# Kernel tuning notes

Measured on AMD Instinct MI355X. Metric: run time of the kernel, lower is better.

Reference implementation:

```python
import jax, jax.numpy as jnp
import numpy as np

B, C, L = 4, 16, 1024
U_SELF, U_CROSS, HID = 32, 16, 128
WIDTH = 128
EPS = 1e-5
LN_EPS = 1e-14


def _band_mask(n, w):
    j = jnp.arange(n)
    lo = j - w // 2
    hi = lo + w
    i = j[:, None]
    return (lo <= i) & (i < hi)  # mask[i, j]: query i attends key j


def _layernorm(x, gamma, beta):
    # channel-first LN over dim 1; gamma/beta shape (C, 1)
    mean = jnp.mean(x, 1, keepdims=True)
    var = jnp.mean((x - mean) ** 2, 1, keepdims=True) + LN_EPS
    return (x - mean) / jnp.sqrt(var) * gamma + beta


def _self_attn(x, Wt, Wx, bh, Wa, ba):
    xt = x.transpose(0, 2, 1)                                # (B,L,C)
    q = xt @ Wt                                              # (B,L,U)
    k = xt @ Wx                                              # (B,L,U)
    h = jnp.tanh(q[:, :, None, :] + k[:, None, :, :] + bh)   # (B,L,L,U)
    e = jnp.squeeze(h @ Wa, -1) + ba                         # (B,L,L)
    e = jnp.exp(e - jnp.max(e, -1, keepdims=True))
    e = jnp.where(_band_mask(e.shape[1], WIDTH), e, 0.0)
    a = e / (jnp.sum(e, -1, keepdims=True) + EPS)
    v = a @ xt                                               # (B,L,C)
    return v.transpose(0, 2, 1)


def _ff(x, W1, b1, W2, b2):
    xt = x.transpose(0, 2, 1)
    h = jax.nn.relu(xt @ W1 + b1)
    return (h @ W2 + b2).transpose(0, 2, 1)


def _transformer(x, Wt, Wx, bh, Wa, ba, g1, be1, W1, b1, W2, b2, g2, be2):
    y = _layernorm(x + _self_attn(x, Wt, Wx, bh, Wa, ba), g1, be1)
    return _layernorm(y + _ff(y, W1, b1, W2, b2), g2, be2)


def _cross(y1, y2, Wq, Wk, Wv):
    y1t = y1.transpose(0, 2, 1)
    y2t = y2.transpose(0, 2, 1)
    q = y1t @ Wq
    k = y2t @ Wk
    v = y2t @ Wv                                             # (B,L,Uc)
    e = (q @ k.transpose(0, 2, 1)) * (1.0 / np.float32(np.sqrt(U_CROSS)))
    e = jnp.where(_band_mask(e.shape[-1], WIDTH), e, -jnp.inf)
    a = jax.nn.softmax(e, -1)
    return (a @ v).transpose(0, 2, 1)                        # (B,Uc,L)


def _forward(x1, x2, t1, t2, cw, top):
    y1 = _transformer(x1, *t1)
    y2 = _transformer(x2, *t2)
    g1, be1, W1, b1, W2, b2, g2, be2 = top
    y = _layernorm(y1 + _cross(y1, y2, *cw), g1, be1)
    return _layernorm(y + _ff(y, W1, b1, W2, b2), g2, be2)


def setup_inputs() -> dict:
    key = jax.random.key(0)
    ks = iter(jax.random.split(key, 64))
    u = lambda shape: jax.random.uniform(next(ks), shape, jnp.float32, -0.02, 0.02)
    n = lambda shape: jax.random.normal(next(ks), shape, jnp.float32) * 0.05
    d = {"x1": jax.random.normal(next(ks), (B, C, L), jnp.float32),
         "x2": jax.random.normal(next(ks), (B, C, L), jnp.float32)}
    for p in ("t1", "t2"):
        d[p + "_Wt"] = u((C, U_SELF)); d[p + "_Wx"] = u((C, U_SELF))
        d[p + "_bh"] = jnp.zeros(U_SELF)
        d[p + "_Wa"] = u((U_SELF, 1)); d[p + "_ba"] = jnp.zeros(1)
        d[p + "_g1"] = jnp.ones((C, 1)); d[p + "_be1"] = jnp.zeros((C, 1))
        d[p + "_W1"] = n((C, HID)); d[p + "_b1"] = jnp.zeros(HID)
        d[p + "_W2"] = n((HID, C)); d[p + "_b2"] = jnp.zeros(C)
        d[p + "_g2"] = jnp.ones((C, 1)); d[p + "_be2"] = jnp.zeros((C, 1))
    d["ca_Wq"] = u((C, U_CROSS)); d["ca_Wk"] = u((C, U_CROSS)); d["ca_Wv"] = u((C, U_CROSS))
    d["g1"] = jnp.ones((C, 1)); d["be1"] = jnp.zeros((C, 1))
    d["W1"] = n((C, HID)); d["b1"] = jnp.zeros(HID)
    d["W2"] = n((HID, C)); d["b2"] = jnp.zeros(C)
    d["g2"] = jnp.ones((C, 1)); d["be2"] = jnp.zeros((C, 1))
    return d


def reference(x1, x2, t1_Wt, t1_Wx, t1_bh, t1_Wa, t1_ba, t1_g1, t1_be1, t1_W1, t1_b1, t1_W2, t1_b2, t1_g2, t1_be2, t2_Wt, t2_Wx, t2_bh, t2_Wa, t2_ba, t2_g1, t2_be1, t2_W1, t2_b1, t2_W2, t2_b2, t2_g2, t2_be2, ca_Wq, ca_Wk, ca_Wv, g1, be1, W1, b1, W2, b2, g2, be2):
    t1 = (t1_Wt, t1_Wx, t1_bh, t1_Wa, t1_ba, t1_g1, t1_be1, t1_W1, t1_b1, t1_W2, t1_b2, t1_g2, t1_be2)
    t2 = (t2_Wt, t2_Wx, t2_bh, t2_Wa, t2_ba, t2_g1, t2_be1, t2_W1, t2_b1, t2_W2, t2_b2, t2_g2, t2_be2)
    cw = (ca_Wq, ca_Wk, ca_Wv)
    top = (g1, be1, W1, b1, W2, b2, g2, be2)
    return _forward(x1, x2, t1, t2, cw, top)
```

## Files before the change

### kernel.cpp

```cpp
#include <hip/hip_runtime.h>
#include <hip/hip_bf16.h>


#define L_    1024
#define C_    16
#define US_   32
#define HID_  128
#define TI1   16
#define TI2   16

struct BranchP {
  const float *x, *Wt, *Wx, *bh, *Wa, *ba, *g1, *be1, *W1, *b1, *W2, *b2, *g2, *be2;
  float* y;
};

__global__ __launch_bounds__(256) void branch_kernel(BranchP Pa, BranchP Pb) {
  const BranchP P = blockIdx.z ? Pb : Pa;
  const int b   = blockIdx.y;
  const int i0  = blockIdx.x * TI1;
  const int tid = threadIdx.x;
  const int j0  = max(0, i0 - 63);
  const int j1  = min(L_, i0 + TI1 + 64);
  const int Wd  = j1 - j0;

  __shared__ float xs[C_][145];
  __shared__ union {
    struct { float ks[144][33]; float qs[TI1][33]; } a;
    struct { float W1s[C_][129]; float W2s[HID_][17]; float b1s[HID_]; } bb;
  } ovl;
  __shared__ float es[TI1][129];
  __shared__ float ya[TI1][17];
  __shared__ float Wts[C_][US_], Wxs[C_][US_];
  __shared__ float m2was[US_], bhs[US_];
  __shared__ float g1s[C_], be1s[C_], b2s[C_], g2s[C_], be2s[C_];
  __shared__ float bas;

  for (int idx = tid; idx < C_ * US_; idx += 256) {
    int c = idx >> 5, u = idx & 31;
    Wts[c][u] = 2.0f * P.Wt[idx];
    Wxs[c][u] = 2.0f * P.Wx[idx];
  }
  if (tid < US_) { m2was[tid] = -2.0f * P.Wa[tid]; bhs[tid] = 2.0f * P.bh[tid]; }
  if (tid < C_) {
    g1s[tid] = P.g1[tid]; be1s[tid] = P.be1[tid];
    g2s[tid] = P.g2[tid]; be2s[tid] = P.be2[tid];
    b2s[tid] = P.b2[tid];
  }
  if (tid == 0) bas = P.ba[0];
  for (int idx = tid; idx < C_ * Wd; idx += 256) {
    int c = idx / Wd, jj = idx - c * Wd;
    xs[c][jj] = P.x[(b * C_ + c) * L_ + j0 + jj];
  }
  __syncthreads();

  for (int idx = tid; idx < Wd * US_; idx += 256) {
    int j = idx >> 5, u = idx & 31;
    float a = bhs[u];
#pragma unroll
    for (int c = 0; c < C_; ++c) a = fmaf(xs[c][j], Wxs[c][u], a);
    ovl.a.ks[j][u] = a;
  }
  for (int idx = tid; idx < TI1 * US_; idx += 256) {
    int i = idx >> 5, u = idx & 31;
    float a = 0.f;
#pragma unroll
    for (int c = 0; c < C_; ++c) a = fmaf(xs[c][i0 - j0 + i], Wts[c][u], a);
    ovl.a.qs[i][u] = a;
  }
  __syncthreads();

  const int il  = tid >> 4, sub = tid & 15;
  const int ig  = i0 + il;
  const int jlo = max(0, ig - 63), jhi = min(L_, ig + 65);
  const int nj  = jhi - jlo;
  const int jb  = jlo - j0;

  float inv;
  {
    float xq[US_];
#pragma unroll
    for (int u = 0; u < US_; ++u) xq[u] = ovl.a.qs[il][u];
    float eacc = bas;
#pragma unroll
    for (int u = 0; u < US_; ++u) eacc -= 0.5f * m2was[u];
    float mx = -1e30f;
    for (int jj = sub; jj < nj; jj += 16) {
      const float* kr = ovl.a.ks[jb + jj];
      float acc = eacc;
#pragma unroll
      for (int u = 0; u < US_; ++u) {
        float t = __expf(xq[u] + kr[u]);
        acc = fmaf(m2was[u], 1.0f / (1.0f + t), acc);
      }
      es[il][jj] = acc;
      mx = fmaxf(mx, acc);
    }
#pragma unroll
    for (int m = 8; m; m >>= 1) mx = fmaxf(mx, __shfl_xor(mx, m));
    float s = 0.f;
    for (int jj = sub; jj < nj; jj += 16) {
      float v = __expf(es[il][jj] - mx);
      es[il][jj] = v; s += v;
    }
#pragma unroll
    for (int m = 8; m; m >>= 1) s += __shfl_xor(s, m);
    inv = 1.0f / (s + 1e-5f);
  }
  __syncthreads();

  for (int idx = tid; idx < C_ * HID_; idx += 256) {
    ovl.bb.W1s[idx >> 7][idx & 127] = P.W1[idx];
    ovl.bb.W2s[idx >> 4][idx & 15]  = P.W2[idx];
  }
  if (tid < HID_) ovl.bb.b1s[tid] = P.b1[tid];
  float yln;
  {
    float v0 = 0.f;
    for (int jj = 0; jj < nj; ++jj) v0 = fmaf(es[il][jj], xs[sub][jb + jj], v0);
    float y0 = xs[sub][ig - j0] + v0 * inv;
    float s1 = y0, s2 = y0 * y0;
#pragma unroll
    for (int m = 8; m; m >>= 1) { s1 += __shfl_xor(s1, m); s2 += __shfl_xor(s2, m); }
    float mean = s1 * (1.f / 16.f);
    float var  = s2 * (1.f / 16.f) - mean * mean;
    float rstd = rsqrtf(fmaxf(var, 0.f) + 1e-14f);
    yln = (y0 - mean) * rstd * g1s[sub] + be1s[sub];
    ya[il][sub] = yln;
  }
  __syncthreads();

  {
    float yc[C_];
#pragma unroll
    for (int c = 0; c < C_; ++c) yc[c] = ya[il][c];
#pragma unroll
    for (int t = 0; t < 8; ++t) {
      int u = sub + 16 * t;
      float a = ovl.bb.b1s[u];
#pragma unroll
      for (int c = 0; c < C_; ++c) a = fmaf(yc[c], ovl.bb.W1s[c][u], a);
      es[il][u] = fmaxf(a, 0.f);
    }
  }
  __syncthreads();

  {
    float o = b2s[sub];
    for (int u = 0; u < HID_; ++u) o = fmaf(es[il][u], ovl.bb.W2s[u][sub], o);
    float y0 = yln + o;
    float s1 = y0, s2 = y0 * y0;
#pragma unroll
    for (int m = 8; m; m >>= 1) { s1 += __shfl_xor(s1, m); s2 += __shfl_xor(s2, m); }
    float mean = s1 * (1.f / 16.f);
    float var  = s2 * (1.f / 16.f) - mean * mean;
    float rstd = rsqrtf(fmaxf(var, 0.f) + 1e-14f);
    P.y[(b * L_ + ig) * C_ + sub] = (y0 - mean) * rstd * g2s[sub] + be2s[sub];
  }
}

__global__ __launch_bounds__(256) void cross_kernel(
    const float* __restrict__ y1g, const float* __restrict__ y2g,
    const float* Wq, const float* Wk, const float* Wv,
    const float* g1, const float* be1, const float* W1, const float* b1,
    const float* W2, const float* b2, const float* g2, const float* be2,
    float* out) {
  const int b   = blockIdx.y;
  const int i0  = blockIdx.x * TI2;
  const int tid = threadIdx.x;
  const int j0  = max(0, i0 - 63);
  const int j1  = min(L_, i0 + TI2 + 64);
  const int Wd  = j1 - j0;

  __shared__ float y1s[TI2][17];
  __shared__ float y2s[144][17];
  __shared__ float Ms[C_][17];
  __shared__ float zs[TI2][17];
  __shared__ float es[TI2][129];
  __shared__ float ya[TI2][17];
  __shared__ float Wqs[C_][C_], Wks[C_][C_], Wvs[C_][C_];
  __shared__ float W1s[C_][129], W2s[HID_][17], b1s[HID_];
  __shared__ float g1s[C_], be1s[C_], b2s[C_], g2s[C_], be2s[C_];

  {
    int c = tid >> 4, u = tid & 15;
    Wqs[c][u] = Wq[tid]; Wks[c][u] = Wk[tid]; Wvs[c][u] = Wv[tid];
    y1s[c][u] = y1g[(b * L_ + i0 + c) * C_ + u];
  }
  for (int idx = tid; idx < C_ * HID_; idx += 256) {
    W1s[idx >> 7][idx & 127] = W1[idx];
    W2s[idx >> 4][idx & 15]  = W2[idx];
  }
  if (tid < HID_) b1s[tid] = b1[tid];
  if (tid < C_) {
    g1s[tid] = g1[tid]; be1s[tid] = be1[tid];
    g2s[tid] = g2[tid]; be2s[tid] = be2[tid];
    b2s[tid] = b2[tid];
  }
  for (int idx = tid; idx < Wd * C_; idx += 256) {
    int jj = idx >> 4, c = idx & 15;
    y2s[jj][c] = y2g[(b * L_ + j0 + jj) * C_ + c];
  }
  __syncthreads();

  {
    int c1 = tid >> 4, c2 = tid & 15;
    float m = 0.f;
#pragma unroll
    for (int u = 0; u < C_; ++u) m = fmaf(Wqs[c1][u], Wks[c2][u], m);
    Ms[c1][c2] = 0.25f * m;
  }
  __syncthreads();
  {
    int i = tid >> 4, c = tid & 15;
    float z = 0.f;
#pragma unroll
    for (int cc = 0; cc < C_; ++cc) z = fmaf(y1s[i][cc], Ms[cc][c], z);
    zs[i][c] = z;
  }
  __syncthreads();

  const int il  = tid >> 4, sub = tid & 15;
  const int ig  = i0 + il;
  const int jlo = max(0, ig - 63), jhi = min(L_, ig + 65);
  const int nj  = jhi - jlo;
  const int jb  = jlo - j0;

  float inv;
  {
    float zr[C_];
#pragma unroll
    for (int c = 0; c < C_; ++c) zr[c] = zs[il][c];
    float mx = -1e30f;
    for (int jj = sub; jj < nj; jj += 16) {
      const float* yr = y2s[jb + jj];
      float a = 0.f;
#pragma unroll
      for (int c = 0; c < C_; ++c) a = fmaf(zr[c], yr[c], a);
      es[il][jj] = a;
      mx = fmaxf(mx, a);
    }
#pragma unroll
    for (int m = 8; m; m >>= 1) mx = fmaxf(mx, __shfl_xor(mx, m));
    float s = 0.f;
    for (int jj = sub; jj < nj; jj += 16) {
      float v = __expf(es[il][jj] - mx);
      es[il][jj] = v; s += v;
    }
#pragma unroll
    for (int m = 8; m; m >>= 1) s += __shfl_xor(s, m);
    inv = 1.0f / s;
  }
  __syncthreads();

  {
    float w = 0.f;
    for (int jj = 0; jj < nj; ++jj) w = fmaf(es[il][jj], y2s[jb + jj][sub], w);
    zs[il][sub] = w * inv;
  }
  __syncthreads();

  float yln;
  {
    float a = 0.f;
#pragma unroll
    for (int c = 0; c < C_; ++c) a = fmaf(zs[il][c], Wvs[c][sub], a);
    float y0 = y1s[il][sub] + a;
    float s1 = y0, s2 = y0 * y0;
#pragma unroll
    for (int m = 8; m; m >>= 1) { s1 += __shfl_xor(s1, m); s2 += __shfl_xor(s2, m); }
    float mean = s1 * (1.f / 16.f);
    float var  = s2 * (1.f / 16.f) - mean * mean;
    float rstd = rsqrtf(fmaxf(var, 0.f) + 1e-14f);
    yln = (y0 - mean) * rstd * g1s[sub] + be1s[sub];
    ya[il][sub] = yln;
  }
  __syncthreads();

  {
    float yc[C_];
#pragma unroll
    for (int c = 0; c < C_; ++c) yc[c] = ya[il][c];
#pragma unroll
    for (int t = 0; t < 8; ++t) {
      int u = sub + 16 * t;
      float a = b1s[u];
#pragma unroll
      for (int c = 0; c < C_; ++c) a = fmaf(yc[c], W1s[c][u], a);
      es[il][u] = fmaxf(a, 0.f);
    }
  }
  __syncthreads();

  {
    float o = b2s[sub];
    for (int u = 0; u < HID_; ++u) o = fmaf(es[il][u], W2s[u][sub], o);
    float y0 = yln + o;
    float s1 = y0, s2 = y0 * y0;
#pragma unroll
    for (int m = 8; m; m >>= 1) { s1 += __shfl_xor(s1, m); s2 += __shfl_xor(s2, m); }
    float mean = s1 * (1.f / 16.f);
    float var  = s2 * (1.f / 16.f) - mean * mean;
    float rstd = rsqrtf(fmaxf(var, 0.f) + 1e-14f);
    es[il][sub] = (y0 - mean) * rstd * g2s[sub] + be2s[sub];
  }
  __syncthreads();

  {
    int c = tid >> 4, i = tid & 15;
    out[(b * C_ + c) * L_ + i0 + i] = es[i][c];
  }
}

extern "C" void kernel_launch(void* const* d_in, const int* in_sizes, int n_in,
                              void* d_out, int out_size, void* d_ws, size_t ws_size,
                              hipStream_t stream) {
  (void)in_sizes; (void)n_in; (void)out_size; (void)ws_size;
  const float* const* in = reinterpret_cast<const float* const*>(d_in);
  float* y1w = reinterpret_cast<float*>(d_ws);
  float* y2w = y1w + 4 * L_ * C_;

  BranchP Pa { in[0],  in[2],  in[3],  in[4],  in[5],  in[6],  in[7],
               in[8],  in[9],  in[10], in[11], in[12], in[13], in[14], y1w };
  BranchP Pb { in[1],  in[15], in[16], in[17], in[18], in[19], in[20],
               in[21], in[22], in[23], in[24], in[25], in[26], in[27], y2w };

  branch_kernel<<<dim3(L_ / TI1, 4, 2), 256, 0, stream>>>(Pa, Pb);
  cross_kernel<<<dim3(L_ / TI2, 4), 256, 0, stream>>>(
      y1w, y2w, in[28], in[29], in[30],
      in[31], in[32], in[33], in[34], in[35], in[36], in[37], in[38],
      reinterpret_cast<float*>(d_out));
}
```

Baseline: 170.8 us.

## Halve query tile, use 32 lanes per query, and use native exp2/rcp

```diff
diff --git a/kernel.cpp b/kernel.cpp
--- a/kernel.cpp
+++ b/kernel.cpp
@@ -1,13 +1,16 @@
 #include <hip/hip_runtime.h>
-#include <hip/hip_bf16.h>
 
 
 #define L_    1024
 #define C_    16
 #define US_   32
 #define HID_  128
-#define TI1   16
-#define TI2   16
+#define TI1   8
+#define TI2   8
+#define K2    2.885390082f
+
+__device__ __forceinline__ float frcp(float x)  { return __builtin_amdgcn_rcpf(x); }
+__device__ __forceinline__ float fexp2(float x) { return __builtin_amdgcn_exp2f(x); }
 
 struct BranchP {
   const float *x, *Wt, *Wx, *bh, *Wa, *ba, *g1, *be1, *W1, *b1, *W2, *b2, *g2, *be2;
@@ -23,9 +26,9 @@
   const int j1  = min(L_, i0 + TI1 + 64);
   const int Wd  = j1 - j0;
 
-  __shared__ float xs[C_][145];
+  __shared__ float xs[C_][137];
   __shared__ union {
-    struct { float ks[144][33]; float qs[TI1][33]; } a;
+    struct { float ks[136][33]; float qs[TI1][33]; } a;
     struct { float W1s[C_][129]; float W2s[HID_][17]; float b1s[HID_]; } bb;
   } ovl;
   __shared__ float es[TI1][129];
@@ -35,12 +38,17 @@
   __shared__ float g1s[C_], be1s[C_], b2s[C_], g2s[C_], be2s[C_];
   __shared__ float bas;
 
+  float w1r[8], w2r[8], b1r = 0.f;
+#pragma unroll
+  for (int t = 0; t < 8; ++t) { w1r[t] = P.W1[tid + 256 * t]; w2r[t] = P.W2[tid + 256 * t]; }
+  if (tid < HID_) b1r = P.b1[tid];
+
   for (int idx = tid; idx < C_ * US_; idx += 256) {
     int c = idx >> 5, u = idx & 31;
-    Wts[c][u] = 2.0f * P.Wt[idx];
-    Wxs[c][u] = 2.0f * P.Wx[idx];
-  }
-  if (tid < US_) { m2was[tid] = -2.0f * P.Wa[tid]; bhs[tid] = 2.0f * P.bh[tid]; }
+    Wts[c][u] = K2 * P.Wt[idx];
+    Wxs[c][u] = K2 * P.Wx[idx];
+  }
+  if (tid < US_) { m2was[tid] = -2.0f * P.Wa[tid]; bhs[tid] = K2 * P.bh[tid]; }
   if (tid < C_) {
     g1s[tid] = P.g1[tid]; be1s[tid] = P.be1[tid];
     g2s[tid] = P.g2[tid]; be2s[tid] = P.be2[tid];
@@ -60,8 +68,8 @@
     for (int c = 0; c < C_; ++c) a = fmaf(xs[c][j], Wxs[c][u], a);
     ovl.a.ks[j][u] = a;
   }
-  for (int idx = tid; idx < TI1 * US_; idx += 256) {
-    int i = idx >> 5, u = idx & 31;
+  {
+    int i = tid >> 5, u = tid & 31;
     float a = 0.f;
 #pragma unroll
     for (int c = 0; c < C_; ++c) a = fmaf(xs[c][i0 - j0 + i], Wts[c][u], a);
@@ -69,11 +77,14 @@
   }
   __syncthreads();
 
-  const int il  = tid >> 4, sub = tid & 15;
-  const int ig  = i0 + il;
-  const int jlo = max(0, ig - 63), jhi = min(L_, ig + 65);
-  const int nj  = jhi - jlo;
-  const int jb  = jlo - j0;
+  const int il   = tid >> 5;
+  const int sub  = tid & 31;
+  const int ig   = i0 + il;
+  const int jlo  = max(0, ig - 63), jhi = min(L_, ig + 65);
+  const int nj   = jhi - jlo;
+  const int jb   = jlo - j0;
+  const int c16  = sub & 15;
+  const int half = sub >> 4;
 
   float inv;
   {
@@ -84,77 +95,83 @@
 #pragma unroll
     for (int u = 0; u < US_; ++u) eacc -= 0.5f * m2was[u];
     float mx = -1e30f;
-    for (int jj = sub; jj < nj; jj += 16) {
+    for (int jj = sub; jj < nj; jj += 32) {
       const float* kr = ovl.a.ks[jb + jj];
       float acc = eacc;
 #pragma unroll
       for (int u = 0; u < US_; ++u) {
-        float t = __expf(xq[u] + kr[u]);
-        acc = fmaf(m2was[u], 1.0f / (1.0f + t), acc);
+        float t = fexp2(xq[u] + kr[u]);
+        acc = fmaf(m2was[u], frcp(1.0f + t), acc);
       }
       es[il][jj] = acc;
       mx = fmaxf(mx, acc);
     }
 #pragma unroll
-    for (int m = 8; m; m >>= 1) mx = fmaxf(mx, __shfl_xor(mx, m));
+    for (int m = 16; m; m >>= 1) mx = fmaxf(mx, __shfl_xor(mx, m));
     float s = 0.f;
-    for (int jj = sub; jj < nj; jj += 16) {
+    for (int jj = sub; jj < nj; jj += 32) {
       float v = __expf(es[il][jj] - mx);
       es[il][jj] = v; s += v;
     }
 #pragma unroll
-    for (int m = 8; m; m >>= 1) s += __shfl_xor(s, m);
-    inv = 1.0f / (s + 1e-5f);
-  }
-  __syncthreads();
-
-  for (int idx = tid; idx < C_ * HID_; idx += 256) {
-    ovl.bb.W1s[idx >> 7][idx & 127] = P.W1[idx];
-    ovl.bb.W2s[idx >> 4][idx & 15]  = P.W2[idx];
-  }
-  if (tid < HID_) ovl.bb.b1s[tid] = P.b1[tid];
+    for (int m = 16; m; m >>= 1) s += __shfl_xor(s, m);
+    inv = frcp(s + 1e-5f);
+  }
+  __syncthreads();
+
+#pragma unroll
+  for (int t = 0; t < 8; ++t) {
+    int idx = tid + 256 * t;
+    ovl.bb.W1s[idx >> 7][idx & 127] = w1r[t];
+  }
+#pragma unroll
+  for (int t = 0; t < 8; ++t) {
+    int idx = tid + 256 * t;
+    ovl.bb.W2s[idx >> 4][idx & 15] = w2r[t];
+  }
+  if (tid < HID_) ovl.bb.b1s[tid] = b1r;
   float yln;
   {
-    float v0 = 0.f;
-    for (int jj = 0; jj < nj; ++jj) v0 = fmaf(es[il][jj], xs[sub][jb + jj], v0);
-    float y0 = xs[sub][ig - j0] + v0 * inv;
+    float v = 0.f;
+    for (int jj = half; jj < nj; jj += 2) v = fmaf(es[il][jj], xs[c16][jb + jj], v);
+    v += __shfl_xor(v, 16);
+    float y0 = xs[c16][ig - j0] + v * inv;
     float s1 = y0, s2 = y0 * y0;
 #pragma unroll
     for (int m = 8; m; m >>= 1) { s1 += __shfl_xor(s1, m); s2 += __shfl_xor(s2, m); }
     float mean = s1 * (1.f / 16.f);
     float var  = s2 * (1.f / 16.f) - mean * mean;
     float rstd = rsqrtf(fmaxf(var, 0.f) + 1e-14f);
-    yln = (y0 - mean) * rstd * g1s[sub] + be1s[sub];
-    ya[il][sub] = yln;
-  }
-  __syncthreads();
-
-  {
-    float yc[C_];
-#pragma unroll
-    for (int c = 0; c < C_; ++c) yc[c] = ya[il][c];
-#pragma unroll
-    for (int t = 0; t < 8; ++t) {
-      int u = sub + 16 * t;
-      float a = ovl.bb.b1s[u];
-#pragma unroll
-      for (int c = 0; c < C_; ++c) a = fmaf(yc[c], ovl.bb.W1s[c][u], a);
-      es[il][u] = fmaxf(a, 0.f);
-    }
-  }
-  __syncthreads();
-
-  {
-    float o = b2s[sub];
-    for (int u = 0; u < HID_; ++u) o = fmaf(es[il][u], ovl.bb.W2s[u][sub], o);
-    float y0 = yln + o;
+    yln = (y0 - mean) * rstd * g1s[c16] + be1s[c16];
+    if (half == 0) ya[il][c16] = yln;
+  }
+  __syncthreads();
+
+#pragma unroll
+  for (int t = 0; t < 4; ++t) {
+    int u = sub + 32 * t;
+    float a = ovl.bb.b1s[u];
+#pragma unroll
+    for (int c = 0; c < C_; ++c) a = fmaf(ya[il][c], ovl.bb.W1s[c][u], a);
+    es[il][u] = fmaxf(a, 0.f);
+  }
+  __syncthreads();
+
+  {
+    float o = 0.f;
+    int u0 = half * 64;
+#pragma unroll
+    for (int uu = 0; uu < 64; ++uu) o = fmaf(es[il][u0 + uu], ovl.bb.W2s[u0 + uu][c16], o);
+    o += __shfl_xor(o, 16);
+    float y0 = yln + o + b2s[c16];
     float s1 = y0, s2 = y0 * y0;
 #pragma unroll
     for (int m = 8; m; m >>= 1) { s1 += __shfl_xor(s1, m); s2 += __shfl_xor(s2, m); }
     float mean = s1 * (1.f / 16.f);
     float var  = s2 * (1.f / 16.f) - mean * mean;
     float rstd = rsqrtf(fmaxf(var, 0.f) + 1e-14f);
-    P.y[(b * L_ + ig) * C_ + sub] = (y0 - mean) * rstd * g2s[sub] + be2s[sub];
+    if (half == 0)
+      P.y[(b * L_ + ig) * C_ + c16] = (y0 - mean) * rstd * g2s[c16] + be2s[c16];
   }
 }
 
@@ -172,7 +189,7 @@
   const int Wd  = j1 - j0;
 
   __shared__ float y1s[TI2][17];
-  __shared__ float y2s[144][17];
+  __shared__ float y2s[136][17];
   __shared__ float Ms[C_][17];
   __shared__ float zs[TI2][17];
   __shared__ float es[TI2][129];
@@ -184,8 +201,9 @@
   {
     int c = tid >> 4, u = tid & 15;
     Wqs[c][u] = Wq[tid]; Wks[c][u] = Wk[tid]; Wvs[c][u] = Wv[tid];
-    y1s[c][u] = y1g[(b * L_ + i0 + c) * C_ + u];
-  }
+  }
+  if (tid < TI2 * C_)
+    y1s[tid >> 4][tid & 15] = y1g[(b * L_ + i0 + (tid >> 4)) * C_ + (tid & 15)];
   for (int idx = tid; idx < C_ * HID_; idx += 256) {
     W1s[idx >> 7][idx & 127] = W1[idx];
     W2s[idx >> 4][idx & 15]  = W2[idx];
@@ -210,7 +228,7 @@
     Ms[c1][c2] = 0.25f * m;
   }
   __syncthreads();
-  {
+  if (tid < TI2 * C_) {
     int i = tid >> 4, c = tid & 15;
     float z = 0.f;
 #pragma unroll
@@ -219,11 +237,14 @@
   }
   __syncthreads();
 
-  const int il  = tid >> 4, sub = tid & 15;
-  const int ig  = i0 + il;
-  const int jlo = max(0, ig - 63), jhi = min(L_, ig + 65);
-  const int nj  = jhi - jlo;
-  const int jb  = jlo - j0;
+  const int il   = tid >> 5;
+  const int sub  = tid & 31;
+  const int ig   = i0 + il;
+  const int jlo  = max(0, ig - 63), jhi = min(L_, ig + 65);
+  const int nj   = jhi - jlo;
+  const int jb   = jlo - j0;
+  const int c16  = sub & 15;
+  const int half = sub >> 4;
 
   float inv;
   {
@@ -231,7 +252,7 @@
 #pragma unroll
     for (int c = 0; c < C_; ++c) zr[c] = zs[il][c];
     float mx = -1e30f;
-    for (int jj = sub; jj < nj; jj += 16) {
+    for (int jj = sub; jj < nj; jj += 32) {
       const float* yr = y2s[jb + jj];
       float a = 0.f;
 #pragma unroll
@@ -240,22 +261,23 @@
       mx = fmaxf(mx, a);
     }
 #pragma unroll
-    for (int m = 8; m; m >>= 1) mx = fmaxf(mx, __shfl_xor(mx, m));
+    for (int m = 16; m; m >>= 1) mx = fmaxf(mx, __shfl_xor(mx, m));
     float s = 0.f;
-    for (int jj = sub; jj < nj; jj += 16) {
+    for (int jj = sub; jj < nj; jj += 32) {
       float v = __expf(es[il][jj] - mx);
       es[il][jj] = v; s += v;
     }
 #pragma unroll
-    for (int m = 8; m; m >>= 1) s += __shfl_xor(s, m);
-    inv = 1.0f / s;
+    for (int m = 16; m; m >>= 1) s += __shfl_xor(s, m);
+    inv = frcp(s);
   }
   __syncthreads();
 
   {
     float w = 0.f;
-    for (int jj = 0; jj < nj; ++jj) w = fmaf(es[il][jj], y2s[jb + jj][sub], w);
-    zs[il][sub] = w * inv;
+    for (int jj = half; jj < nj; jj += 2) w = fmaf(es[il][jj], y2s[jb + jj][c16], w);
+    w += __shfl_xor(w, 16);
+    if (half == 0) zs[il][c16] = w * inv;
   }
   __syncthreads();
 
@@ -263,51 +285,49 @@
   {
     float a = 0.f;
 #pragma unroll
-    for (int c = 0; c < C_; ++c) a = fmaf(zs[il][c], Wvs[c][sub], a);
-    float y0 = y1s[il][sub] + a;
+    for (int c = 0; c < C_; ++c) a = fmaf(zs[il][c], Wvs[c][c16], a);
+    float y0 = y1s[il][c16] + a;
     float s1 = y0, s2 = y0 * y0;
 #pragma unroll
     for (int m = 8; m; m >>= 1) { s1 += __shfl_xor(s1, m); s2 += __shfl_xor(s2, m); }
     float mean = s1 * (1.f / 16.f);
     float var  = s2 * (1.f / 16.f) - mean * mean;
     float rstd = rsqrtf(fmaxf(var, 0.f) + 1e-14f);
-    yln = (y0 - mean) * rstd * g1s[sub] + be1s[sub];
-    ya[il][sub] = yln;
-  }
-  __syncthreads();
-
-  {
-    float yc[C_];
-#pragma unroll
-    for (int c = 0; c < C_; ++c) yc[c] = ya[il][c];
-#pragma unroll
-    for (int t = 0; t < 8; ++t) {
-      int u = sub + 16 * t;
-      float a = b1s[u];
-#pragma unroll
-      for (int c = 0; c < C_; ++c) a = fmaf(yc[c], W1s[c][u], a);
-      es[il][u] = fmaxf(a, 0.f);
-    }
-  }
-  __syncthreads();
-
-  {
-    float o = b2s[sub];
-    for (int u = 0; u < HID_; ++u) o = fmaf(es[il][u], W2s[u][sub], o);
-    float y0 = yln + o;
+    yln = (y0 - mean) * rstd * g1s[c16] + be1s[c16];
+    if (half == 0) ya[il][c16] = yln;
+  }
+  __syncthreads();
+
+#pragma unroll
+  for (int t = 0; t < 4; ++t) {
+    int u = sub + 32 * t;
+    float a = b1s[u];
+#pragma unroll
+    for (int c = 0; c < C_; ++c) a = fmaf(ya[il][c], W1s[c][u], a);
+    es[il][u] = fmaxf(a, 0.f);
+  }
+  __syncthreads();
+
+  {
+    float o = 0.f;
+    int u0 = half * 64;
+#pragma unroll
+    for (int uu = 0; uu < 64; ++uu) o = fmaf(es[il][u0 + uu], W2s[u0 + uu][c16], o);
+    o += __shfl_xor(o, 16);
+    float y0 = yln + o + b2s[c16];
     float s1 = y0, s2 = y0 * y0;
 #pragma unroll
     for (int m = 8; m; m >>= 1) { s1 += __shfl_xor(s1, m); s2 += __shfl_xor(s2, m); }
     float mean = s1 * (1.f / 16.f);
     float var  = s2 * (1.f / 16.f) - mean * mean;
     float rstd = rsqrtf(fmaxf(var, 0.f) + 1e-14f);
-    es[il][sub] = (y0 - mean) * rstd * g2s[sub] + be2s[sub];
-  }
-  __syncthreads();
-
-  {
-    int c = tid >> 4, i = tid & 15;
-    out[(b * C_ + c) * L_ + i0 + i] = es[i][c];
+    if (half == 0) zs[il][c16] = (y0 - mean) * rstd * g2s[c16] + be2s[c16];
+  }
+  __syncthreads();
+
+  if (tid < C_ * TI2) {
+    int c = tid >> 3, i = tid & 7;
+    out[(b * C_ + c) * L_ + i0 + i] = zs[i][c];
   }
 }
 
```

After: 172.3 us. Within noise of the previous version (+0.9%).
